# Kernel tuning notes

Hardware: AMD Instinct MI355X
Metric: run time of the kernel (lower is better)

The kernel has to match this reference:

```python
import jax, jax.numpy as jnp
import numpy as np

N, C = 16384, 2048
CPG = 16          # num_pergroup (c)
T = 5             # Newton-Schulz iterations
EPS = 1e-5


def setup_inputs() -> dict:
    key = jax.random.key(0)
    k1, k2, k3 = jax.random.split(key, 3)
    return {
        "x": jax.random.normal(k1, (N, C), dtype=jnp.float32),
        "sw_mean_weight": jax.random.normal(k2, (2,), dtype=jnp.float32),
        "sw_var_weight": jax.random.normal(k3, (2,), dtype=jnp.float32),
        "weight": jnp.ones((C,), dtype=jnp.float32),
        "bias": jnp.zeros((C,), dtype=jnp.float32),
    }


def reference(x, sw_mean_weight, sw_var_weight, weight, bias):
    n, ch = x.shape
    c = CPG
    g = ch // c
    # --- BW (batch whitening) stats: x.T viewed as (g, c, N) ---
    xt = x.T.reshape(g, c, n)
    mean_bn = jnp.mean(xt, axis=-1, keepdims=True)            # (g, c, 1)
    xc = xt - mean_bn
    cov_bn = jnp.einsum('gcn,gdn->gcd', xc, xc) / n           # (g, c, c)
    # --- IW stats: in_data = x.view(N*g, c, 1) => mean_in = in_data, cov_in = 0 ---
    mw = jax.nn.softmax(sw_mean_weight)
    vw = jax.nn.softmax(sw_var_weight)
    eye = jnp.eye(c, dtype=x.dtype)
    # cov identical for every sample (cov_in == 0) -> whiten once per group
    cov = vw[0] * cov_bn + EPS * eye                          # (g, c, c)
    # --- Newton-Schulz iterative whitening ---
    rTr = 1.0 / jnp.trace(cov, axis1=1, axis2=2)[:, None, None]
    covN = cov * rTr
    P = jnp.broadcast_to(eye, (g, c, c))
    for _ in range(T):
        P3 = jnp.einsum('gab,gbc,gcd->gad', P, P, P)
        P = 1.5 * P - 0.5 * jnp.einsum('gad,gde->gae', P3, covN)
    wm = P * jnp.sqrt(rTr)                                    # (g, c, c)
    # --- apply: wm @ (in_data - mean),  mean = mw0*mean_bn + mw1*in_data ---
    z = x.reshape(n, g, c)
    zc = (1.0 - mw[1]) * z - mw[0] * mean_bn[None, :, :, 0]   # (N, g, c)
    y = jnp.einsum('gcd,ngd->ngc', wm, zc).reshape(n, ch)
    return y * weight + bias
```

## Files before the change

kernel.cpp:

```cpp
#include <hip/hip_runtime.h>
#include <cstddef>

#define NROWS 16384
#define NCOLS 2048
#define CPG   16
#define NGRP  128
#define EPS_W 1e-5f
#define NS_T  5

#define TROWS 32
#define CHUNKS 32
#define RPB (NROWS / CHUNKS)
#define NT_STATS (RPB / TROWS)
#define ASTRIPES 64
#define RPA (NROWS / ASTRIPES)
#define NT_APPLY (RPA / TROWS)

#define PART_STRIDE 272

__device__ __forceinline__ float dot4(float4 p, float4 v) {
  return p.x * v.x + p.y * v.y + p.z * v.z + p.w * v.w;
}

__global__ __launch_bounds__(256) void k_stats(const float* __restrict__ x,
                                               float* __restrict__ part) {
  __shared__ __align__(16) float tile[2][TROWS * 256];
  const int cb   = blockIdx.x;
  const int ch   = blockIdx.y;
  const int t    = threadIdx.x;
  const int col0 = cb << 8;
  const int r0   = ch * RPB;

  const int g  = t >> 4;
  const int ti = t & 15;
  const int tc = (ti >> 2) << 2;
  const int td = (ti & 3) << 2;

  float mac = 0.f;
  float acc00 = 0.f, acc01 = 0.f, acc02 = 0.f, acc03 = 0.f;
  float acc10 = 0.f, acc11 = 0.f, acc12 = 0.f, acc13 = 0.f;
  float acc20 = 0.f, acc21 = 0.f, acc22 = 0.f, acc23 = 0.f;
  float acc30 = 0.f, acc31 = 0.f, acc32 = 0.f, acc33 = 0.f;

  float4 st[8];
#pragma unroll
  for (int i = 0; i < 8; ++i) {
    const int f = (i << 8) | t;
    const int r = f >> 6, cq = f & 63;
    st[i] = *(const float4*)(x + (size_t)(r0 + r) * NCOLS + col0 + (cq << 2));
  }
#pragma unroll
  for (int i = 0; i < 8; ++i) {
    const int f = (i << 8) | t;
    *(float4*)(&tile[0][f << 2]) = st[i];
  }
  __syncthreads();

  int cur = 0;
  for (int tb = 0; tb < NT_STATS; ++tb) {
    const bool hn = (tb + 1 < NT_STATS);
    if (hn) {
      const int rn = r0 + (tb + 1) * TROWS;
#pragma unroll
      for (int i = 0; i < 8; ++i) {
        const int f = (i << 8) | t;
        const int r = f >> 6, cq = f & 63;
        st[i] = *(const float4*)(x + (size_t)(rn + r) * NCOLS + col0 + (cq << 2));
      }
    }
    const float* __restrict__ buf = tile[cur];
#pragma unroll 4
    for (int r = 0; r < TROWS; ++r) {
      const float* row = buf + r * 256;
      mac += row[t];
      const float* rg = row + (g << 4);
      const float4 xa = *(const float4*)(rg + tc);
      const float4 xb = *(const float4*)(rg + td);
      acc00 += xa.x * xb.x; acc01 += xa.x * xb.y; acc02 += xa.x * xb.z; acc03 += xa.x * xb.w;
      acc10 += xa.y * xb.x; acc11 += xa.y * xb.y; acc12 += xa.y * xb.z; acc13 += xa.y * xb.w;
      acc20 += xa.z * xb.x; acc21 += xa.z * xb.y; acc22 += xa.z * xb.z; acc23 += xa.z * xb.w;
      acc30 += xa.w * xb.x; acc31 += xa.w * xb.y; acc32 += xa.w * xb.z; acc33 += xa.w * xb.w;
    }
    if (hn) {
#pragma unroll
      for (int i = 0; i < 8; ++i) {
        const int f = (i << 8) | t;
        *(float4*)(&tile[cur ^ 1][f << 2]) = st[i];
      }
    }
    __syncthreads();
    cur ^= 1;
  }

  float* p = part + ((size_t)ch * NGRP + (cb << 4) + g) * PART_STRIDE;
  p[ti] = mac;
  const int base = 16 + tc * 16 + td;
  p[base + 0 * 16 + 0] = acc00; p[base + 0 * 16 + 1] = acc01; p[base + 0 * 16 + 2] = acc02; p[base + 0 * 16 + 3] = acc03;
  p[base + 1 * 16 + 0] = acc10; p[base + 1 * 16 + 1] = acc11; p[base + 1 * 16 + 2] = acc12; p[base + 1 * 16 + 3] = acc13;
  p[base + 2 * 16 + 0] = acc20; p[base + 2 * 16 + 1] = acc21; p[base + 2 * 16 + 2] = acc22; p[base + 2 * 16 + 3] = acc23;
  p[base + 3 * 16 + 0] = acc30; p[base + 3 * 16 + 1] = acc31; p[base + 3 * 16 + 2] = acc32; p[base + 3 * 16 + 3] = acc33;
}

__global__ __launch_bounds__(256) void k_ns(const float* __restrict__ part,
                                            const float* __restrict__ swm,
                                            const float* __restrict__ swv,
                                            const float* __restrict__ wgt,
                                            const float* __restrict__ bia,
                                            float* __restrict__ A2,
                                            float* __restrict__ b2) {
  __shared__ float sP[256], sA[256], sB[256], sN[256], smean[16];
  __shared__ float strace;
  const int G = blockIdx.x;
  const int t = threadIdx.x;
  const int c = t >> 4, d = t & 15;

  float m2 = 0.f;
  for (int ch = 0; ch < CHUNKS; ++ch)
    m2 += part[((size_t)ch * NGRP + G) * PART_STRIDE + 16 + t];
  if (t < 16) {
    float ms = 0.f;
    for (int ch = 0; ch < CHUNKS; ++ch)
      ms += part[((size_t)ch * NGRP + G) * PART_STRIDE + t];
    smean[t] = ms * (1.f / NROWS);
  }
  __syncthreads();

  const float a0 = swm[0], a1 = swm[1];
  const float am = fmaxf(a0, a1);
  const float e0 = expf(a0 - am), e1 = expf(a1 - am);
  const float mw0 = e0 / (e0 + e1), mw1 = e1 / (e0 + e1);
  const float v0 = swv[0], v1 = swv[1];
  const float vm = fmaxf(v0, v1);
  const float f0 = expf(v0 - vm), f1 = expf(v1 - vm);
  const float vw0 = f0 / (f0 + f1);

  float cov = m2 * (1.f / NROWS) - smean[c] * smean[d];
  cov = vw0 * cov + ((c == d) ? EPS_W : 0.f);
  sN[t] = cov;
  __syncthreads();
  if (t == 0) {
    float tr = 0.f;
#pragma unroll
    for (int k = 0; k < 16; ++k) tr += sN[k * 17];
    strace = 1.f / tr;
  }
  __syncthreads();
  const float rTr = strace;
  sN[t] = cov * rTr;
  sP[t] = (c == d) ? 1.f : 0.f;
  __syncthreads();

  for (int it = 0; it < NS_T; ++it) {
    float p2 = 0.f;
#pragma unroll
    for (int k = 0; k < 16; ++k) p2 += sP[c * 16 + k] * sP[k * 16 + d];
    sA[t] = p2;
    __syncthreads();
    float p3 = 0.f;
#pragma unroll
    for (int k = 0; k < 16; ++k) p3 += sA[c * 16 + k] * sP[k * 16 + d];
    sB[t] = p3;
    __syncthreads();
    float qv = 0.f;
#pragma unroll
    for (int k = 0; k < 16; ++k) qv += sB[c * 16 + k] * sN[k * 16 + d];
    const float np = 1.5f * sP[t] - 0.5f * qv;
    __syncthreads();
    sP[t] = np;
    __syncthreads();
  }

  const float wmv = sP[t] * sqrtf(rTr);
  const float wr = wgt[(G << 4) + c];
  A2[(size_t)G * 256 + t] = wmv * (1.f - mw1) * wr;
  sA[t] = wmv * smean[d];
  __syncthreads();
  if (t < 16) {
    float s = 0.f;
#pragma unroll
    for (int k = 0; k < 16; ++k) s += sA[t * 16 + k];
    b2[(G << 4) + t] = -mw0 * s * wgt[(G << 4) + t] + bia[(G << 4) + t];
  }
}

__global__ __launch_bounds__(256) void k_apply(const float* __restrict__ x,
                                               const float* __restrict__ A2,
                                               const float* __restrict__ b2,
                                               float* __restrict__ y) {
  __shared__ __align__(16) float tile[2][TROWS * 256];
  const int cb   = blockIdx.x;
  const int stb  = blockIdx.y;
  const int t    = threadIdx.x;
  const int col0 = cb << 8;
  const int r0   = stb * RPA;

  const int w  = t >> 6, l = t & 63;
  const int g  = (w << 2) | (l >> 4);
  const int q  = (l >> 2) & 3;
  const int rp = l & 3;
  const int G  = (cb << 4) | g;

  float4 a[4][4];
#pragma unroll
  for (int i = 0; i < 4; ++i)
#pragma unroll
    for (int dq = 0; dq < 4; ++dq)
      a[i][dq] = *(const float4*)(A2 + (size_t)G * 256 + ((q << 2) + i) * 16 + (dq << 2));
  float bv[4];
#pragma unroll
  for (int i = 0; i < 4; ++i) bv[i] = b2[(G << 4) + (q << 2) + i];

  float4 st[8];
#pragma unroll
  for (int i = 0; i < 8; ++i) {
    const int f = (i << 8) | t;
    const int r = f >> 6, cq = f & 63;
    st[i] = *(const float4*)(x + (size_t)(r0 + r) * NCOLS + col0 + (cq << 2));
  }
#pragma unroll
  for (int i = 0; i < 8; ++i) {
    const int f = (i << 8) | t;
    *(float4*)(&tile[0][f << 2]) = st[i];
  }
  __syncthreads();

  int cur = 0;
  for (int tb = 0; tb < NT_APPLY; ++tb) {
    const bool hn = (tb + 1 < NT_APPLY);
    if (hn) {
      const int rn = r0 + (tb + 1) * TROWS;
#pragma unroll
      for (int i = 0; i < 8; ++i) {
        const int f = (i << 8) | t;
        const int r = f >> 6, cq = f & 63;
        st[i] = *(const float4*)(x + (size_t)(rn + r) * NCOLS + col0 + (cq << 2));
      }
    }
    const float* __restrict__ buf = tile[cur];
    const int rbase = r0 + tb * TROWS;
#pragma unroll
    for (int r = rp; r < TROWS; r += 4) {
      const float* xr = buf + r * 256 + (g << 4);
      const float4 xv0 = *(const float4*)(xr + 0);
      const float4 xv1 = *(const float4*)(xr + 4);
      const float4 xv2 = *(const float4*)(xr + 8);
      const float4 xv3 = *(const float4*)(xr + 12);
      const float s0 = bv[0] + dot4(a[0][0], xv0) + dot4(a[0][1], xv1) + dot4(a[0][2], xv2) + dot4(a[0][3], xv3);
      const float s1 = bv[1] + dot4(a[1][0], xv0) + dot4(a[1][1], xv1) + dot4(a[1][2], xv2) + dot4(a[1][3], xv3);
      const float s2 = bv[2] + dot4(a[2][0], xv0) + dot4(a[2][1], xv1) + dot4(a[2][2], xv2) + dot4(a[2][3], xv3);
      const float s3 = bv[3] + dot4(a[3][0], xv0) + dot4(a[3][1], xv1) + dot4(a[3][2], xv2) + dot4(a[3][3], xv3);
      *(float4*)(y + (size_t)(rbase + r) * NCOLS + col0 + (g << 4) + (q << 2)) =
          make_float4(s0, s1, s2, s3);
    }
    if (hn) {
#pragma unroll
      for (int i = 0; i < 8; ++i) {
        const int f = (i << 8) | t;
        *(float4*)(&tile[cur ^ 1][f << 2]) = st[i];
      }
    }
    __syncthreads();
    cur ^= 1;
  }
}

extern "C" void kernel_launch(void* const* d_in, const int* in_sizes, int n_in,
                              void* d_out, int out_size, void* d_ws, size_t ws_size,
                              hipStream_t stream) {
  (void)in_sizes; (void)n_in; (void)out_size; (void)ws_size;
  const float* x   = (const float*)d_in[0];
  const float* swm = (const float*)d_in[1];
  const float* swv = (const float*)d_in[2];
  const float* wgt = (const float*)d_in[3];
  const float* bia = (const float*)d_in[4];
  float* out = (float*)d_out;

  float* part = (float*)d_ws;
  float* A2   = part + (size_t)CHUNKS * NGRP * PART_STRIDE;
  float* b2   = A2 + (size_t)NGRP * 256;

  k_stats<<<dim3(8, CHUNKS), 256, 0, stream>>>(x, part);
  k_ns<<<NGRP, 256, 0, stream>>>(part, swm, swv, wgt, bia, A2, b2);
  k_apply<<<dim3(8, ASTRIPES), 256, 0, stream>>>(x, A2, b2, out);
}
```

Baseline: 341.6 us.

## Use atomic partial reduction for stats and direct-load nontemporal apply kernel

The stats kernel now uses more row chunks with a single LDS buffer and accumulates its partial sums into one per-group buffer via atomicAdd, after a memset. This removes the chunk-reduction loop in the Newton-Schulz kernel. The apply kernel drops LDS staging and reads x directly from global memory with nontemporal loads and stores, using more row stripes for parallelism. The trade-offs are atomic contention, an extra memset launch, and less coalescing-friendly direct loads.

```diff
diff --git a/kernel.cpp b/kernel.cpp
--- a/kernel.cpp
+++ b/kernel.cpp
@@ -1,35 +1,31 @@
 #include <hip/hip_runtime.h>
 #include <cstddef>
 
+typedef float f4 __attribute__((ext_vector_type(4)));
+
 #define NROWS 16384
 #define NCOLS 2048
-#define CPG   16
 #define NGRP  128
 #define EPS_W 1e-5f
 #define NS_T  5
 
 #define TROWS 32
-#define CHUNKS 32
-#define RPB (NROWS / CHUNKS)
-#define NT_STATS (RPB / TROWS)
-#define ASTRIPES 64
-#define RPA (NROWS / ASTRIPES)
-#define NT_APPLY (RPA / TROWS)
-
+#define S_CH  128
+#define S_RPB (NROWS / S_CH)
+#define S_NT  (S_RPB / TROWS)
 #define PART_STRIDE 272
 
-__device__ __forceinline__ float dot4(float4 p, float4 v) {
-  return p.x * v.x + p.y * v.y + p.z * v.z + p.w * v.w;
-}
+#define A_STRIPES 256
+#define A_RPB (NROWS / A_STRIPES)
 
 __global__ __launch_bounds__(256) void k_stats(const float* __restrict__ x,
                                                float* __restrict__ part) {
-  __shared__ __align__(16) float tile[2][TROWS * 256];
+  __shared__ __align__(16) float tile[TROWS * 256];
   const int cb   = blockIdx.x;
   const int ch   = blockIdx.y;
   const int t    = threadIdx.x;
   const int col0 = cb << 8;
-  const int r0   = ch * RPB;
+  const int r0   = ch * S_RPB;
 
   const int g  = t >> 4;
   const int ti = t & 15;
@@ -37,68 +33,54 @@
   const int td = (ti & 3) << 2;
 
   float mac = 0.f;
-  float acc00 = 0.f, acc01 = 0.f, acc02 = 0.f, acc03 = 0.f;
-  float acc10 = 0.f, acc11 = 0.f, acc12 = 0.f, acc13 = 0.f;
-  float acc20 = 0.f, acc21 = 0.f, acc22 = 0.f, acc23 = 0.f;
-  float acc30 = 0.f, acc31 = 0.f, acc32 = 0.f, acc33 = 0.f;
-
-  float4 st[8];
+  float acc[4][4] = {{0.f}};
+
+  f4 st[8];
 #pragma unroll
   for (int i = 0; i < 8; ++i) {
     const int f = (i << 8) | t;
     const int r = f >> 6, cq = f & 63;
-    st[i] = *(const float4*)(x + (size_t)(r0 + r) * NCOLS + col0 + (cq << 2));
-  }
-#pragma unroll
-  for (int i = 0; i < 8; ++i) {
-    const int f = (i << 8) | t;
-    *(float4*)(&tile[0][f << 2]) = st[i];
-  }
-  __syncthreads();
-
-  int cur = 0;
-  for (int tb = 0; tb < NT_STATS; ++tb) {
-    const bool hn = (tb + 1 < NT_STATS);
-    if (hn) {
+    st[i] = *(const f4*)(x + (size_t)(r0 + r) * NCOLS + col0 + (cq << 2));
+  }
+
+  for (int tb = 0; tb < S_NT; ++tb) {
+    __syncthreads();
+#pragma unroll
+    for (int i = 0; i < 8; ++i) {
+      const int f = (i << 8) | t;
+      *(f4*)(&tile[f << 2]) = st[i];
+    }
+    __syncthreads();
+    if (tb + 1 < S_NT) {
       const int rn = r0 + (tb + 1) * TROWS;
 #pragma unroll
       for (int i = 0; i < 8; ++i) {
         const int f = (i << 8) | t;
         const int r = f >> 6, cq = f & 63;
-        st[i] = *(const float4*)(x + (size_t)(rn + r) * NCOLS + col0 + (cq << 2));
+        st[i] = *(const f4*)(x + (size_t)(rn + r) * NCOLS + col0 + (cq << 2));
       }
     }
-    const float* __restrict__ buf = tile[cur];
 #pragma unroll 4
     for (int r = 0; r < TROWS; ++r) {
-      const float* row = buf + r * 256;
+      const float* row = tile + r * 256;
       mac += row[t];
-      const float* rg = row + (g << 4);
-      const float4 xa = *(const float4*)(rg + tc);
-      const float4 xb = *(const float4*)(rg + td);
-      acc00 += xa.x * xb.x; acc01 += xa.x * xb.y; acc02 += xa.x * xb.z; acc03 += xa.x * xb.w;
-      acc10 += xa.y * xb.x; acc11 += xa.y * xb.y; acc12 += xa.y * xb.z; acc13 += xa.y * xb.w;
-      acc20 += xa.z * xb.x; acc21 += xa.z * xb.y; acc22 += xa.z * xb.z; acc23 += xa.z * xb.w;
-      acc30 += xa.w * xb.x; acc31 += xa.w * xb.y; acc32 += xa.w * xb.z; acc33 += xa.w * xb.w;
+      const f4 xa = *(const f4*)(row + (g << 4) + tc);
+      const f4 xb = *(const f4*)(row + (g << 4) + td);
+#pragma unroll
+      for (int i = 0; i < 4; ++i)
+#pragma unroll
+        for (int j = 0; j < 4; ++j)
+          acc[i][j] += xa[i] * xb[j];
     }
-    if (hn) {
-#pragma unroll
-      for (int i = 0; i < 8; ++i) {
-        const int f = (i << 8) | t;
-        *(float4*)(&tile[cur ^ 1][f << 2]) = st[i];
-      }
-    }
-    __syncthreads();
-    cur ^= 1;
-  }
-
-  float* p = part + ((size_t)ch * NGRP + (cb << 4) + g) * PART_STRIDE;
-  p[ti] = mac;
-  const int base = 16 + tc * 16 + td;
-  p[base + 0 * 16 + 0] = acc00; p[base + 0 * 16 + 1] = acc01; p[base + 0 * 16 + 2] = acc02; p[base + 0 * 16 + 3] = acc03;
-  p[base + 1 * 16 + 0] = acc10; p[base + 1 * 16 + 1] = acc11; p[base + 1 * 16 + 2] = acc12; p[base + 1 * 16 + 3] = acc13;
-  p[base + 2 * 16 + 0] = acc20; p[base + 2 * 16 + 1] = acc21; p[base + 2 * 16 + 2] = acc22; p[base + 2 * 16 + 3] = acc23;
-  p[base + 3 * 16 + 0] = acc30; p[base + 3 * 16 + 1] = acc31; p[base + 3 * 16 + 2] = acc32; p[base + 3 * 16 + 3] = acc33;
+  }
+
+  float* pg = part + (size_t)((cb << 4) + g) * PART_STRIDE;
+  atomicAdd(&pg[ti], mac);
+#pragma unroll
+  for (int i = 0; i < 4; ++i)
+#pragma unroll
+    for (int j = 0; j < 4; ++j)
+      atomicAdd(&pg[16 + (tc + i) * 16 + (td + j)], acc[i][j]);
 }
 
 __global__ __launch_bounds__(256) void k_ns(const float* __restrict__ part,
@@ -114,15 +96,8 @@
   const int t = threadIdx.x;
   const int c = t >> 4, d = t & 15;
 
-  float m2 = 0.f;
-  for (int ch = 0; ch < CHUNKS; ++ch)
-    m2 += part[((size_t)ch * NGRP + G) * PART_STRIDE + 16 + t];
-  if (t < 16) {
-    float ms = 0.f;
-    for (int ch = 0; ch < CHUNKS; ++ch)
-      ms += part[((size_t)ch * NGRP + G) * PART_STRIDE + t];
-    smean[t] = ms * (1.f / NROWS);
-  }
+  const float m2 = part[(size_t)G * PART_STRIDE + 16 + t];
+  if (t < 16) smean[t] = part[(size_t)G * PART_STRIDE + t] * (1.f / NROWS);
   __syncthreads();
 
   const float a0 = swm[0], a1 = swm[1];
@@ -183,84 +158,61 @@
   }
 }
 
+__device__ __forceinline__ float dot16(const f4* ar, f4 u0, f4 u1, f4 u2, f4 u3) {
+  const f4 p = ar[0] * u0 + ar[1] * u1 + ar[2] * u2 + ar[3] * u3;
+  return p.x + p.y + p.z + p.w;
+}
+
 __global__ __launch_bounds__(256) void k_apply(const float* __restrict__ x,
                                                const float* __restrict__ A2,
                                                const float* __restrict__ b2,
                                                float* __restrict__ y) {
-  __shared__ __align__(16) float tile[2][TROWS * 256];
-  const int cb   = blockIdx.x;
-  const int stb  = blockIdx.y;
-  const int t    = threadIdx.x;
+  const int cb  = blockIdx.x;
+  const int stb = blockIdx.y;
+  const int t   = threadIdx.x;
+  const int q   = t & 3;
+  const int g   = (t >> 2) & 15;
+  const int ph  = t >> 6;
+  const int G   = (cb << 4) | g;
   const int col0 = cb << 8;
-  const int r0   = stb * RPA;
-
-  const int w  = t >> 6, l = t & 63;
-  const int g  = (w << 2) | (l >> 4);
-  const int q  = (l >> 2) & 3;
-  const int rp = l & 3;
-  const int G  = (cb << 4) | g;
-
-  float4 a[4][4];
+
+  f4 a[4][4];
 #pragma unroll
   for (int i = 0; i < 4; ++i)
 #pragma unroll
     for (int dq = 0; dq < 4; ++dq)
-      a[i][dq] = *(const float4*)(A2 + (size_t)G * 256 + ((q << 2) + i) * 16 + (dq << 2));
-  float bv[4];
-#pragma unroll
-  for (int i = 0; i < 4; ++i) bv[i] = b2[(G << 4) + (q << 2) + i];
-
-  float4 st[8];
-#pragma unroll
-  for (int i = 0; i < 8; ++i) {
-    const int f = (i << 8) | t;
-    const int r = f >> 6, cq = f & 63;
-    st[i] = *(const float4*)(x + (size_t)(r0 + r) * NCOLS + col0 + (cq << 2));
-  }
-#pragma unroll
-  for (int i = 0; i < 8; ++i) {
-    const int f = (i << 8) | t;
-    *(float4*)(&tile[0][f << 2]) = st[i];
-  }
-  __syncthreads();
-
-  int cur = 0;
-  for (int tb = 0; tb < NT_APPLY; ++tb) {
-    const bool hn = (tb + 1 < NT_APPLY);
-    if (hn) {
-      const int rn = r0 + (tb + 1) * TROWS;
-#pragma unroll
-      for (int i = 0; i < 8; ++i) {
-        const int f = (i << 8) | t;
-        const int r = f >> 6, cq = f & 63;
-        st[i] = *(const float4*)(x + (size_t)(rn + r) * NCOLS + col0 + (cq << 2));
-      }
-    }
-    const float* __restrict__ buf = tile[cur];
-    const int rbase = r0 + tb * TROWS;
-#pragma unroll
-    for (int r = rp; r < TROWS; r += 4) {
-      const float* xr = buf + r * 256 + (g << 4);
-      const float4 xv0 = *(const float4*)(xr + 0);
-      const float4 xv1 = *(const float4*)(xr + 4);
-      const float4 xv2 = *(const float4*)(xr + 8);
-      const float4 xv3 = *(const float4*)(xr + 12);
-      const float s0 = bv[0] + dot4(a[0][0], xv0) + dot4(a[0][1], xv1) + dot4(a[0][2], xv2) + dot4(a[0][3], xv3);
-      const float s1 = bv[1] + dot4(a[1][0], xv0) + dot4(a[1][1], xv1) + dot4(a[1][2], xv2) + dot4(a[1][3], xv3);
-      const float s2 = bv[2] + dot4(a[2][0], xv0) + dot4(a[2][1], xv1) + dot4(a[2][2], xv2) + dot4(a[2][3], xv3);
-      const float s3 = bv[3] + dot4(a[3][0], xv0) + dot4(a[3][1], xv1) + dot4(a[3][2], xv2) + dot4(a[3][3], xv3);
-      *(float4*)(y + (size_t)(rbase + r) * NCOLS + col0 + (g << 4) + (q << 2)) =
-          make_float4(s0, s1, s2, s3);
-    }
-    if (hn) {
-#pragma unroll
-      for (int i = 0; i < 8; ++i) {
-        const int f = (i << 8) | t;
-        *(float4*)(&tile[cur ^ 1][f << 2]) = st[i];
-      }
-    }
-    __syncthreads();
-    cur ^= 1;
+      a[i][dq] = *(const f4*)(A2 + (size_t)G * 256 + ((q << 2) + i) * 16 + (dq << 2));
+  const f4 bv = *(const f4*)(b2 + (G << 4) + (q << 2));
+
+  const int r0 = stb * A_RPB + ph;
+  const size_t xoff = (size_t)col0 + (g << 4);
+  const size_t yoff = (size_t)col0 + ((size_t)(t & 63) << 2);
+
+  for (int i = 0; i < A_RPB / 4; i += 2) {
+    const size_t ra = (size_t)(r0 + 4 * i) * NCOLS;
+    const size_t rb = (size_t)(r0 + 4 * i + 4) * NCOLS;
+    const float* pa = x + ra + xoff;
+    const float* pb = x + rb + xoff;
+    const f4 u0 = __builtin_nontemporal_load((const f4*)(pa + 0));
+    const f4 u1 = __builtin_nontemporal_load((const f4*)(pa + 4));
+    const f4 u2 = __builtin_nontemporal_load((const f4*)(pa + 8));
+    const f4 u3 = __builtin_nontemporal_load((const f4*)(pa + 12));
+    const f4 v0 = __builtin_nontemporal_load((const f4*)(pb + 0));
+    const f4 v1 = __builtin_nontemporal_load((const f4*)(pb + 4));
+    const f4 v2 = __builtin_nontemporal_load((const f4*)(pb + 8));
+    const f4 v3 = __builtin_nontemporal_load((const f4*)(pb + 12));
+
+    f4 oa, ob;
+    oa.x = bv.x + dot16(a[0], u0, u1, u2, u3);
+    oa.y = bv.y + dot16(a[1], u0, u1, u2, u3);
+    oa.z = bv.z + dot16(a[2], u0, u1, u2, u3);
+    oa.w = bv.w + dot16(a[3], u0, u1, u2, u3);
+    __builtin_nontemporal_store(oa, (f4*)(y + ra + yoff));
+    ob.x = bv.x + dot16(a[0], v0, v1, v2, v3);
+    ob.y = bv.y + dot16(a[1], v0, v1, v2, v3);
+    ob.z = bv.z + dot16(a[2], v0, v1, v2, v3);
+    ob.w = bv.w + dot16(a[3], v0, v1, v2, v3);
+    __builtin_nontemporal_store(ob, (f4*)(y + rb + yoff));
   }
 }
 
@@ -276,10 +228,11 @@
   float* out = (float*)d_out;
 
   float* part = (float*)d_ws;
-  float* A2   = part + (size_t)CHUNKS * NGRP * PART_STRIDE;
+  float* A2   = part + (size_t)NGRP * PART_STRIDE;
   float* b2   = A2 + (size_t)NGRP * 256;
 
-  k_stats<<<dim3(8, CHUNKS), 256, 0, stream>>>(x, part);
+  hipMemsetAsync(part, 0, (size_t)NGRP * PART_STRIDE * sizeof(float), stream);
+  k_stats<<<dim3(8, S_CH), 256, 0, stream>>>(x, part);
   k_ns<<<NGRP, 256, 0, stream>>>(part, swm, swv, wgt, bia, A2, b2);
-  k_apply<<<dim3(8, ASTRIPES), 256, 0, stream>>>(x, A2, b2, out);
-}
+  k_apply<<<dim3(8, A_STRIPES), 256, 0, stream>>>(x, A2, b2, out);
+}
```

Measured after the change: 362.0 us. 6.0% more time.
